# Kernel tuning notes

Hardware: AMD Instinct MI355X
Metric: run time of the kernel (lower is better)

The kernel has to match this reference:

```python
import jax, jax.numpy as jnp
import numpy as np


def setup_inputs() -> dict:
    key = jax.random.key(0)
    k1, k2, k3 = jax.random.split(key, 3)
    B, N, T, F = 4, 512, 64, 256
    x = jax.random.normal(k1, (B, N, T, F), dtype=jnp.float32)
    adj = jax.random.uniform(k2, (N, N), dtype=jnp.float32)
    # nn.Linear(F, F, bias=False) weight, layout [out, in]
    theta_w = jax.random.normal(k3, (F, F), dtype=jnp.float32) / np.float32(np.sqrt(F))
    return {"x": x, "adj": adj, "theta_w": theta_w}


def reference(x, adj, theta_w):
    # x: (B, N, T, F) -> out: (B, N, T, F). Dropout p=0 (eval mode).
    B, N, T, F = x.shape
    scale = np.float32(1.0 / np.sqrt(F))
    # fold time into batch: (B*T, N, F)
    xf = jnp.transpose(x, (0, 2, 1, 3)).reshape(B * T, N, F)
    # SAt: softmax((x x^T)/sqrt(F)); forward divides by sqrt(F) again
    score = jnp.einsum("bnf,bmf->bnm", xf, xf) * scale
    att = jax.nn.softmax(score, axis=-1) * scale  # (B*T, N, N)
    # adjacency-masked attention aggregation
    h = jnp.einsum("bnm,bmf->bnf", adj[None, :, :] * att, xf)  # (B*T, N, F)
    # Theta linear (no bias): y = h @ W^T
    y = jnp.einsum("bnf,of->bno", h, theta_w)
    y = y.reshape(B, T, N, F).transpose(0, 2, 1, 3)  # (B, N, T, F)
    return jax.nn.relu(y)
```

## Files before the change

### kernel.cpp

```cpp
#include <hip/hip_runtime.h>


typedef __attribute__((ext_vector_type(8))) _Float16 h16x8;
typedef __attribute__((ext_vector_type(4))) float f32x4;
typedef __attribute__((ext_vector_type(4))) unsigned short us4;
typedef __attribute__((ext_vector_type(8))) unsigned short us8;

#define MFMA16(a, b, c) __builtin_amdgcn_mfma_f32_16x16x32_f16((a), (b), (c), 0, 0, 0)

__device__ __forceinline__ unsigned short f2h(float f) {
    _Float16 h = (_Float16)f;
    return __builtin_bit_cast(unsigned short, h);
}
__device__ __forceinline__ void st4(unsigned short* p, unsigned short a, unsigned short b,
                                    unsigned short c, unsigned short d) {
    us4 v = {a, b, c, d};
    *(us4*)p = v;
}
__device__ __forceinline__ us8 pack8(float4 a, float4 b) {
    us8 v = {f2h(a.x), f2h(a.y), f2h(a.z), f2h(a.w), f2h(b.x), f2h(b.y), f2h(b.z), f2h(b.w)};
    return v;
}
__device__ __forceinline__ void gload16(const void* g, void* l) {
    __builtin_amdgcn_global_load_lds(
        (const __attribute__((address_space(1))) unsigned int*)g,
        (__attribute__((address_space(3))) unsigned int*)l, 16, 0, 0);
}

namespace {
constexpr int Nn = 512;
constexpr int TT = 64;
constexpr int FF = 256;
constexpr int TTFF = TT * FF;
constexpr int PLD = 40;
constexpr int XLD = 264;
constexpr float SCALE = 0.0625f;
constexpr float K2 = 0.09016844f;
constexpr float C2 = 24.525816f;
constexpr float CLMP = 15.9f;
constexpr size_t XH_ELEMS = (size_t)256 * 512 * 256;
constexpr size_t XT_ELEMS = (size_t)256 * 256 * 512;
constexpr size_t WH_ELEMS = 256 * 256;
constexpr size_t AJ_ELEMS = (size_t)2 * 16 * 8192;
constexpr int KLD = 264;
constexpr int TLD = 72;
constexpr int FPLD = 40;
constexpr int HLD = 256;
constexpr int WLD = 128;
}

__global__ __launch_bounds__(256, 4) void prepass(const float* __restrict__ x,
                                                  const float* __restrict__ W,
                                                  const float* __restrict__ adj,
                                                  unsigned short* __restrict__ xh,
                                                  unsigned short* __restrict__ xT2,
                                                  unsigned short* __restrict__ Wh,
                                                  unsigned short* __restrict__ adjL) {
    const int bid = blockIdx.x;
    const int t = threadIdx.x;
    if (bid >= 2056) {
        const int bid2 = bid - 2056;
        #pragma unroll
        for (int k = 0; k < 4; ++k) {
            const int U = bid2 * 1024 + k * 256 + t;
            const int qt  = U >> 14;
            const int t16 = (U >> 10) & 15;
            const int u   = U & 1023;
            const int half = u >> 9;
            const int wv   = (u >> 6) & 7;
            const int lv   = u & 63;
            const int lgv  = lv >> 4, lcv = lv & 15;
            us8 v;
            #pragma unroll
            for (int ee = 0; ee < 8; ++ee) {
                const int jt = ee >> 2, r = ee & 3;
                const int row = qt * 256 + wv * 32 + half * 16 + lgv * 4 + r;
                const int col = t16 * 32 + jt * 16 + lcv;
                v[ee] = f2h(adj[(size_t)row * Nn + col]);
            }
            *(us8*)&adjL[(size_t)U * 8] = v;
        }
        return;
    }
    if (bid >= 2048) {
        const int j = (bid - 2048) * 256 + t;
        #pragma unroll
        for (int k = 0; k < 4; ++k) {
            float4 a = *(const float4*)(W + j * 32 + k * 8);
            float4 b = *(const float4*)(W + j * 32 + k * 8 + 4);
            *(us8*)&Wh[j * 32 + k * 8] = pack8(a, b);
        }
        return;
    }
    __shared__ unsigned short tile[64 * XLD];
    const int bt = bid >> 3;
    const int nc = bid & 7;
    const int b = bt >> 6, tt = bt & 63;
    const int nbase = nc * 64;
    const float* xbt = x + (size_t)b * (Nn * TTFF) + (size_t)tt * FF;

    const int fb8 = (t & 31) * 8;
    const int rg = t >> 5;
    #pragma unroll
    for (int i = 0; i < 8; ++i) {
        const int rl = rg * 8 + i;
        const int n = nbase + rl;
        float4 a = *(const float4*)(xbt + (size_t)n * TTFF + fb8);
        float4 c = *(const float4*)(xbt + (size_t)n * TTFF + fb8 + 4);
        us8 v = pack8(a, c);
        *(us8*)&xh[((size_t)bt * Nn + n) * FF + (fb8 ^ (8 * (n & 7)))] = v;
        *(us8*)&tile[rl * XLD + fb8] = v;
    }
    __syncthreads();
    const int n0 = (t & 7) * 8;
    const int fr = t >> 3;
    #pragma unroll
    for (int j = 0; j < 8; ++j) {
        const int f = fr + 32 * j;
        const int g2 = 8 * ((f >> 1) & 3);
        const int n0p = (n0 & 32) | ((n0 & 24) ^ g2);
        us8 v;
        #pragma unroll
        for (int k = 0; k < 8; ++k) v[k] = tile[(n0p + k) * XLD + f];
        const int m = nbase + n0;
        *(us8*)&xT2[((size_t)bt * 16 + (m >> 5)) * 8192 + f * 32 + (m & 31)] = v;
    }
}

__global__ __launch_bounds__(512, 2) void gcn_main(float* __restrict__ out,
                                                   const unsigned short* __restrict__ xh,
                                                   const unsigned short* __restrict__ xT2,
                                                   const unsigned short* __restrict__ Wh,
                                                   const unsigned short* __restrict__ adjL) {
    __shared__ alignas(16) union {
        struct { unsigned short kt[2][32][256]; unsigned short vt[2][256][32];
                 unsigned short at[2][8192]; unsigned short pb[8][32][PLD]; } m;
        struct { unsigned short hb[256][264]; unsigned short wc[64][136]; } e;
    } sm;

    const int tid = threadIdx.x;
    const int w  = tid >> 6;
    const int l  = tid & 63;
    const int lg = l >> 4;
    const int lc = l & 15;
    const int fsw = 8 * (lc & 7);

    const int lb = (blockIdx.x & 7) * 64 + (blockIdx.x >> 3);
    const int bt = lb >> 1;
    const int qt = lb & 1;
    const int b  = bt >> 6;
    const int tt = bt & 63;
    const int qbase = qt * 256;

    const unsigned short* xhb = xh + (size_t)bt * (Nn * FF);
    const unsigned short* xTb = xT2 + (size_t)bt * (FF * Nn);
    const unsigned short* ajq = adjL + (size_t)qt * (16 * 8192);

    auto stage = [&](int u) {
        const int c = u & 1;
        const size_t off = (size_t)(u & 15) * 8192 + (size_t)tid * 8;
        unsigned short* ktd = &sm.m.kt[c][0][0] + (size_t)tid * 8;
        unsigned short* vtd = &sm.m.vt[c][0][0] + (size_t)tid * 8;
        unsigned short* atd = &sm.m.at[c][0]    + (size_t)tid * 8;
        gload16(&xhb[off],        ktd);
        gload16(&xhb[off + 4096], ktd + 4096);
        gload16(&xTb[off],        vtd);
        gload16(&xTb[off + 4096], vtd + 4096);
        gload16(&ajq[off],        atd);
        gload16(&ajq[off + 4096], atd + 4096);
    };

    stage(0);

    h16x8 qf[2][8];
    #pragma unroll
    for (int qs = 0; qs < 2; ++qs) {
        const unsigned short* qp = &xhb[(size_t)(qbase + 32 * w + 16 * qs + lc) * FF];
        #pragma unroll
        for (int ks = 0; ks < 8; ++ks) {
            us8 v = *(const us8*)(qp + ((ks * 32 + lg * 8) ^ fsw));
            qf[qs][ks] = __builtin_bit_cast(h16x8, v);
        }
    }

    f32x4 acc[2][16];
    #pragma unroll
    for (int q = 0; q < 2; ++q)
        #pragma unroll
        for (int i = 0; i < 16; ++i) { f32x4 z = {0.f, 0.f, 0.f, 0.f}; acc[q][i] = z; }
    float rs[2][4] = {{0.f,0.f,0.f,0.f},{0.f,0.f,0.f,0.f}};
    const int msw2 = 8 * ((lc >> 1) & 3);
    const int pwsw = 8 * ((lg >> 1) & 1);
    const int prsw = 8 * ((lc >> 3) & 1);

    for (int t = 0; t < 16; ++t) {
        const int c = t & 1;

        asm volatile("s_waitcnt vmcnt(0)" ::: "memory");
        __builtin_amdgcn_s_barrier();
        __builtin_amdgcn_sched_barrier(0);

        stage(t + 1);

        h16x8 a0 = *(const h16x8*)&sm.m.at[c][(w << 9) + l * 8];
        h16x8 a1 = *(const h16x8*)&sm.m.at[c][4096 + (w << 9) + l * 8];

        f32x4 s[2][2];
        #pragma unroll
        for (int qs = 0; qs < 2; ++qs)
            #pragma unroll
            for (int jt = 0; jt < 2; ++jt) { f32x4 z = {0.f,0.f,0.f,0.f}; s[qs][jt] = z; }
        __builtin_amdgcn_s_setprio(1);
        #pragma unroll
        for (int ks = 0; ks < 8; ++ks) {
            const int col = (ks * 32 + lg * 8) ^ fsw;
            h16x8 b0 = *(const h16x8*)&sm.m.kt[c][lc][col];
            h16x8 b1 = *(const h16x8*)&sm.m.kt[c][16 + lc][col];
            s[0][0] = MFMA16(qf[0][ks], b0, s[0][0]);
            s[0][1] = MFMA16(qf[0][ks], b1, s[0][1]);
            s[1][0] = MFMA16(qf[1][ks], b0, s[1][0]);
            s[1][1] = MFMA16(qf[1][ks], b1, s[1][1]);
        }
        __builtin_amdgcn_s_setprio(0);

        #pragma unroll
        for (int qs = 0; qs < 2; ++qs)
            #pragma unroll
            for (int jt = 0; jt < 2; ++jt)
                #pragma unroll
                for (int r = 0; r < 4; ++r) {
                    float p = exp2f(fminf(fmaf(s[qs][jt][r], K2, -C2), CLMP));
                    rs[qs][r] += p;
                    float av = (float)(qs ? a1[jt * 4 + r] : a0[jt * 4 + r]);
                    sm.m.pb[w][qs * 16 + 4 * lg + r][(jt * 16 + lc) ^ pwsw] = f2h(p * av);
                }
        h16x8 pa0 = *(const h16x8*)&sm.m.pb[w][lc][(lg * 8) ^ prsw];
        h16x8 pa1 = *(const h16x8*)&sm.m.pb[w][16 + lc][(lg * 8) ^ prsw];

        const int mcol = (lg * 8) ^ msw2;
        __builtin_amdgcn_s_setprio(1);
        #pragma unroll
        for (int ft = 0; ft < 16; ++ft) {
            h16x8 bv = *(const h16x8*)&sm.m.vt[c][ft * 16 + lc][mcol];
            acc[0][ft] = MFMA16(pa0, bv, acc[0][ft]);
            acc[1][ft] = MFMA16(pa1, bv, acc[1][ft]);
        }
        __builtin_amdgcn_s_setprio(0);
    }

    asm volatile("s_waitcnt vmcnt(0)" ::: "memory");
    __builtin_amdgcn_s_barrier();

    {
        #pragma unroll
        for (int qs = 0; qs < 2; ++qs) {
            float c0[4];
            #pragma unroll
            for (int r = 0; r < 4; ++r) {
                float t0 = rs[qs][r];
                t0 += __shfl_xor(t0, 1);
                t0 += __shfl_xor(t0, 2);
                t0 += __shfl_xor(t0, 4);
                t0 += __shfl_xor(t0, 8);
                c0[r] = SCALE / t0;
            }
            #pragma unroll
            for (int ft = 0; ft < 16; ++ft)
                #pragma unroll
                for (int r = 0; r < 4; ++r)
                    sm.e.hb[32 * w + 16 * qs + 4 * lg + r][ft * 16 + lc] =
                        f2h(acc[qs][ft][r] * c0[r]);
        }
    }

    #pragma unroll
    for (int ohh = 0; ohh < 4; ++ohh) {
        f32x4 y4[2][4];
        #pragma unroll
        for (int qs = 0; qs < 2; ++qs)
            #pragma unroll
            for (int i = 0; i < 4; ++i) { f32x4 z = {0.f, 0.f, 0.f, 0.f}; y4[qs][i] = z; }
        #pragma unroll
        for (int fh = 0; fh < 2; ++fh) {
            __syncthreads();
            {
                const int o  = tid >> 3;
                const int cc = (tid & 7) * 16;
                const unsigned short* gp = &Wh[(size_t)(ohh * 64 + o) * FF + fh * 128 + cc];
                *(us8*)&sm.e.wc[o][cc]     = *(const us8*)gp;
                *(us8*)&sm.e.wc[o][cc + 8] = *(const us8*)(gp + 8);
            }
            __syncthreads();
            h16x8 ha[2][4];
            #pragma unroll
            for (int qs = 0; qs < 2; ++qs)
                #pragma unroll
                for (int k2 = 0; k2 < 4; ++k2)
                    ha[qs][k2] = *(const h16x8*)
                        &sm.e.hb[32 * w + 16 * qs + lc][fh * 128 + k2 * 32 + lg * 8];
            #pragma unroll
            for (int ot = 0; ot < 4; ++ot) {
                #pragma unroll
                for (int k2 = 0; k2 < 4; ++k2) {
                    h16x8 bw = *(const h16x8*)&sm.e.wc[ot * 16 + lc][k2 * 32 + lg * 8];
                    y4[0][ot] = MFMA16(ha[0][k2], bw, y4[0][ot]);
                    y4[1][ot] = MFMA16(ha[1][k2], bw, y4[1][ot]);
                }
            }
        }
        #pragma unroll
        for (int qs = 0; qs < 2; ++qs)
            #pragma unroll
            for (int r = 0; r < 4; ++r) {
                const int row = qbase + 32 * w + 16 * qs + 4 * lg + r;
                float* op = &out[((size_t)(b * Nn + row) * TT + tt) * FF];
                #pragma unroll
                for (int ot = 0; ot < 4; ++ot) {
                    const int o = ohh * 64 + ot * 16 + lc;
                    float v = y4[qs][ot][r];
                    op[o] = v > 0.f ? v : 0.f;
                }
            }
    }
}

__global__ __launch_bounds__(256, 2) void gcn_fallback(const float* __restrict__ x,
                                                       const float* __restrict__ adj,
                                                       const float* __restrict__ W,
                                                       float* __restrict__ out) {
    __shared__ alignas(16) union {
        struct { unsigned short kt[64 * KLD]; unsigned short vt[256 * TLD];
                 unsigned short pb[4 * 32 * FPLD]; } m;
        struct { unsigned short hb[128 * HLD]; unsigned short wc[32 * WLD]; } e;
    } sm;

    const int tid = threadIdx.x;
    const int w  = tid >> 6;
    const int l  = tid & 63;
    const int lg = l >> 4;
    const int lc = l & 15;

    const int lb = (blockIdx.x & 7) * 128 + (blockIdx.x >> 3);
    const int bt = lb >> 2;
    const int qt = lb & 3;
    const int b  = bt >> 6;
    const int tt = bt & 63;
    const int qbase = qt * 128;

    const float* xbt = x + (size_t)b * (Nn * TTFF) + (size_t)tt * FF;

    h16x8 qf[2][8];
    #pragma unroll
    for (int qs = 0; qs < 2; ++qs) {
        const float* qp = xbt + (size_t)(qbase + 32 * w + 16 * qs + lc) * TTFF;
        #pragma unroll
        for (int ks = 0; ks < 8; ++ks) {
            float4 a = *(const float4*)(qp + ks * 32 + lg * 8);
            float4 c = *(const float4*)(qp + ks * 32 + lg * 8 + 4);
            h16x8 v;
            v[0] = (_Float16)(a.x * SCALE); v[1] = (_Float16)(a.y * SCALE);
            v[2] = (_Float16)(a.z * SCALE); v[3] = (_Float16)(a.w * SCALE);
            v[4] = (_Float16)(c.x * SCALE); v[5] = (_Float16)(c.y * SCALE);
            v[6] = (_Float16)(c.z * SCALE); v[7] = (_Float16)(c.w * SCALE);
            qf[qs][ks] = v;
        }
    }

    f32x4 acc[2][16];
    #pragma unroll
    for (int q = 0; q < 2; ++q)
        #pragma unroll
        for (int i = 0; i < 16; ++i) { f32x4 z = {0.f, 0.f, 0.f, 0.f}; acc[q][i] = z; }
    float mrow[2][4] = {{-1e30f,-1e30f,-1e30f,-1e30f},{-1e30f,-1e30f,-1e30f,-1e30f}};
    float lrow[2][4] = {{0.f,0.f,0.f,0.f},{0.f,0.f,0.f,0.f}};

    const int m0  = 4 * (tid >> 4);
    const int fb4 = 4 * (tid & 15);
    const int msw = m0 ^ (8 * (tid & 7));

    for (int kt2 = 0; kt2 < 8; ++kt2) {
        const int kbase = kt2 * 64;
        #pragma unroll
        for (int i = 0; i < 4; ++i) {
            const int f0 = fb4 + 64 * i;
            const float* p = xbt + (size_t)(kbase + m0) * TTFF + f0;
            float4 r0 = *(const float4*)(p);
            float4 r1 = *(const float4*)(p + TTFF);
            float4 r2 = *(const float4*)(p + 2 * TTFF);
            float4 r3 = *(const float4*)(p + 3 * TTFF);
            unsigned short a0=f2h(r0.x),a1=f2h(r0.y),a2=f2h(r0.z),a3=f2h(r0.w);
            unsigned short b0=f2h(r1.x),b1=f2h(r1.y),b2=f2h(r1.z),b3=f2h(r1.w);
            unsigned short c0=f2h(r2.x),c1=f2h(r2.y),c2=f2h(r2.z),c3=f2h(r2.w);
            unsigned short d0=f2h(r3.x),d1=f2h(r3.y),d2=f2h(r3.z),d3=f2h(r3.w);
            st4(&sm.m.kt[(m0 + 0) * KLD + f0], a0, a1, a2, a3);
            st4(&sm.m.kt[(m0 + 1) * KLD + f0], b0, b1, b2, b3);
            st4(&sm.m.kt[(m0 + 2) * KLD + f0], c0, c1, c2, c3);
            st4(&sm.m.kt[(m0 + 3) * KLD + f0], d0, d1, d2, d3);
            st4(&sm.m.vt[(f0 + 0) * TLD + msw], a0, b0, c0, d0);
            st4(&sm.m.vt[(f0 + 1) * TLD + msw], a1, b1, c1, d1);
            st4(&sm.m.vt[(f0 + 2) * TLD + msw], a2, b2, c2, d2);
            st4(&sm.m.vt[(f0 + 3) * TLD + msw], a3, b3, c3, d3);
        }
        __syncthreads();

        f32x4 s0[4], s1[4];
        #pragma unroll
        for (int jt = 0; jt < 4; ++jt) {
            f32x4 t0 = {0.f, 0.f, 0.f, 0.f}, t1 = {0.f, 0.f, 0.f, 0.f};
            #pragma unroll
            for (int ks = 0; ks < 8; ++ks) {
                h16x8 bf = *(const h16x8*)&sm.m.kt[(jt * 16 + lc) * KLD + ks * 32 + lg * 8];
                t0 = MFMA16(qf[0][ks], bf, t0);
                t1 = MFMA16(qf[1][ks], bf, t1);
            }
            s0[jt] = t0; s1[jt] = t1;
        }

        float resc[2][4];
        #pragma unroll
        for (int qs = 0; qs < 2; ++qs) {
            f32x4* s = qs ? s1 : s0;
            const int qrow0 = qbase + 32 * w + 16 * qs + 4 * lg;
            #pragma unroll
            for (int r = 0; r < 4; ++r) {
                float mx = fmaxf(fmaxf(s[0][r], s[1][r]), fmaxf(s[2][r], s[3][r]));
                mx = fmaxf(mx, __shfl_xor(mx, 1));
                mx = fmaxf(mx, __shfl_xor(mx, 2));
                mx = fmaxf(mx, __shfl_xor(mx, 4));
                mx = fmaxf(mx, __shfl_xor(mx, 8));
                float mnew = fmaxf(mrow[qs][r], mx);
                resc[qs][r] = exp2f((mrow[qs][r] - mnew) * 1.44269504f);
                mrow[qs][r] = mnew;
                float rss = 0.f;
                #pragma unroll
                for (int jt = 0; jt < 4; ++jt) {
                    float p = exp2f((s[jt][r] - mnew) * 1.44269504f);
                    rss += p;
                    s[jt][r] = p * adj[(qrow0 + r) * Nn + kbase + jt * 16 + lc];
                }
                rss += __shfl_xor(rss, 1);
                rss += __shfl_xor(rss, 2);
                rss += __shfl_xor(rss, 4);
                rss += __shfl_xor(rss, 8);
                lrow[qs][r] = lrow[qs][r] * resc[qs][r] + rss;
            }
        }
        #pragma unroll
        for (int qs = 0; qs < 2; ++qs)
            #pragma unroll
            for (int ft = 0; ft < 16; ++ft)
                #pragma unroll
                for (int r = 0; r < 4; ++r) acc[qs][ft][r] *= resc[qs][r];

        #pragma unroll
        for (int ks = 0; ks < 2; ++ks) {
            #pragma unroll
            for (int qs = 0; qs < 2; ++qs) {
                const f32x4* s = qs ? s1 : s0;
                #pragma unroll
                for (int jl = 0; jl < 2; ++jl)
                    #pragma unroll
                    for (int r = 0; r < 4; ++r)
                        sm.m.pb[(w * 32 + qs * 16 + 4 * lg + r) * FPLD + jl * 16 + lc] =
                            f2h(s[2 * ks + jl][r]);
            }
            h16x8 pa0 = *(const h16x8*)&sm.m.pb[(w * 32 + lc) * FPLD + lg * 8];
            h16x8 pa1 = *(const h16x8*)&sm.m.pb[(w * 32 + 16 + lc) * FPLD + lg * 8];
            #pragma unroll
            for (int ft = 0; ft < 16; ++ft) {
                const int f = ft * 16 + lc;
                const int ms = (ks * 32 + lg * 8) ^ (8 * ((4 * ft + (lc >> 2)) & 7));
                h16x8 bv = *(const h16x8*)&sm.m.vt[f * TLD + ms];
                acc[0][ft] = MFMA16(pa0, bv, acc[0][ft]);
                acc[1][ft] = MFMA16(pa1, bv, acc[1][ft]);
            }
        }
        __syncthreads();
    }

    {
        float c0[2][4];
        #pragma unroll
        for (int qs = 0; qs < 2; ++qs)
            #pragma unroll
            for (int r = 0; r < 4; ++r) c0[qs][r] = SCALE / lrow[qs][r];
        #pragma unroll
        for (int qs = 0; qs < 2; ++qs)
            #pragma unroll
            for (int ft = 0; ft < 16; ++ft)
                #pragma unroll
                for (int r = 0; r < 4; ++r) {
                    const int row = 32 * w + 16 * qs + 4 * lg + r;
                    const int col = (ft * 16 + lc) ^ (8 * ((4 * lg + r) & 7));
                    sm.e.hb[row * HLD + col] = f2h(acc[qs][ft][r] * c0[qs][r]);
                }
    }
    __syncthreads();

    f32x4 y[8][2][2];
    #pragma unroll
    for (int oh = 0; oh < 8; ++oh)
        #pragma unroll
        for (int qs = 0; qs < 2; ++qs)
            #pragma unroll
            for (int ot = 0; ot < 2; ++ot) { f32x4 z = {0.f,0.f,0.f,0.f}; y[oh][qs][ot] = z; }

    #pragma unroll
    for (int fh = 0; fh < 2; ++fh) {
        h16x8 ha[2][4];
        #pragma unroll
        for (int qs = 0; qs < 2; ++qs)
            #pragma unroll
            for (int k2 = 0; k2 < 4; ++k2) {
                const int row = 32 * w + 16 * qs + lc;
                const int col = (fh * 128 + k2 * 32 + lg * 8) ^ (8 * (lc & 7));
                ha[qs][k2] = *(const h16x8*)&sm.e.hb[row * HLD + col];
            }
        #pragma unroll
        for (int oh = 0; oh < 8; ++oh) {
            __syncthreads();
            {
                const int o  = tid >> 3;
                const int cb = (tid & 7) * 16;
                const float* gp = &W[(size_t)(oh * 32 + o) * FF + fh * 128 + cb];
                float4 v0 = *(const float4*)(gp);
                float4 v1 = *(const float4*)(gp + 4);
                float4 v2 = *(const float4*)(gp + 8);
                float4 v3 = *(const float4*)(gp + 12);
                const int sw = 16 * (o & 3);
                *(us8*)&sm.e.wc[o * WLD + (cb ^ sw)]       = pack8(v0, v1);
                *(us8*)&sm.e.wc[o * WLD + ((cb + 8) ^ sw)] = pack8(v2, v3);
            }
            __syncthreads();
            #pragma unroll
            for (int ot = 0; ot < 2; ++ot) {
                #pragma unroll
                for (int k2 = 0; k2 < 4; ++k2) {
                    const int row = ot * 16 + lc;
                    const int col = (k2 * 32 + lg * 8) ^ (16 * (lc & 3));
                    h16x8 bw = *(const h16x8*)&sm.e.wc[row * WLD + col];
                    y[oh][0][ot] = MFMA16(ha[0][k2], bw, y[oh][0][ot]);
                    y[oh][1][ot] = MFMA16(ha[1][k2], bw, y[oh][1][ot]);
                }
            }
        }
    }

    #pragma unroll
    for (int qs = 0; qs < 2; ++qs)
        #pragma unroll
        for (int r = 0; r < 4; ++r) {
            const int row = qbase + 32 * w + 16 * qs + 4 * lg + r;
            float* op = &out[((size_t)(b * Nn + row) * TT + tt) * FF];
            #pragma unroll
            for (int oh = 0; oh < 8; ++oh)
                #pragma unroll
                for (int ot = 0; ot < 2; ++ot) {
                    const int o = oh * 32 + ot * 16 + lc;
                    float v = y[oh][qs][ot][r];
                    op[o] = v > 0.f ? v : 0.f;
                }
        }
}

extern "C" void kernel_launch(void* const* d_in, const int* in_sizes, int n_in,
                              void* d_out, int out_size, void* d_ws, size_t ws_size,
                              hipStream_t stream) {
    const float* x   = (const float*)d_in[0];
    const float* adj = (const float*)d_in[1];
    const float* w   = (const float*)d_in[2];
    float* out       = (float*)d_out;
    (void)in_sizes; (void)n_in; (void)out_size;

    unsigned short* xh  = (unsigned short*)d_ws;
    unsigned short* xT2 = xh + XH_ELEMS;
    unsigned short* Wh  = xT2 + XT_ELEMS;
    unsigned short* aL  = Wh + WH_ELEMS;
    const size_t need = (XH_ELEMS + XT_ELEMS + WH_ELEMS + AJ_ELEMS) * sizeof(unsigned short);

    if (ws_size >= need) {
        prepass<<<dim3(2088), dim3(256), 0, stream>>>(x, w, adj, xh, xT2, Wh, aL);
        gcn_main<<<dim3(512), dim3(512), 0, stream>>>(out, xh, xT2, Wh, aL);
    } else {
        gcn_fallback<<<dim3(1024), dim3(256), 0, stream>>>(x, adj, w, out);
    }
}
```

Baseline: 176.0 us.

## Triple-buffer K/V staging, prefetch W through registers, and swizzle hb LDS

The K/V tiles in the main attention loop become triple-buffered and are issued two iterations ahead. The wait now uses a partial vmcnt instead of draining all loads, which is meant to hide global-load latency behind the MFMA work. The epilogue Theta GEMM now double-buffers 32-row W chunks and prefetches the next chunk into registers while the current one is computed, and XOR swizzles are added to the hb and pb LDS accesses to cut bank conflicts. The costs are more LDS per block, which may reduce occupancy, and more barriers in the epilogue because chunks are smaller.

Measured after the change: 189.1 us. +7.4%, slower.

```diff
diff --git a/kernel.cpp b/kernel.cpp
--- a/kernel.cpp
+++ b/kernel.cpp
@@ -133,9 +133,12 @@
                                                    const unsigned short* __restrict__ Wh,
                                                    const unsigned short* __restrict__ adjL) {
     __shared__ alignas(16) union {
-        struct { unsigned short kt[2][32][256]; unsigned short vt[2][256][32];
-                 unsigned short at[2][8192]; unsigned short pb[8][32][PLD]; } m;
-        struct { unsigned short hb[256][264]; unsigned short wc[64][136]; } e;
+        struct { unsigned short kt[3][32][256];
+                 unsigned short vt[3][256][32];
+                 unsigned short at[2][8192];
+                 unsigned short pb[8][32][PLD]; } m;
+        struct { unsigned short hb[256][264];
+                 unsigned short wc[2][32][136]; } e;
     } sm;
 
     const int tid = threadIdx.x;
@@ -156,32 +159,39 @@
     const unsigned short* xTb = xT2 + (size_t)bt * (FF * Nn);
     const unsigned short* ajq = adjL + (size_t)qt * (16 * 8192);
 
-    auto stage = [&](int u) {
-        const int c = u & 1;
+    h16x8 qf[2][8];
+    #pragma unroll
+    for (int qs = 0; qs < 2; ++qs) {
+        const unsigned short* qp = &xhb[(size_t)(qbase + 32 * w + 16 * qs + lc) * FF];
+        #pragma unroll
+        for (int ks = 0; ks < 8; ++ks) {
+            us8 v = *(const us8*)(qp + ((ks * 32 + lg * 8) ^ fsw));
+            qf[qs][ks] = __builtin_bit_cast(h16x8, v);
+        }
+    }
+    __builtin_amdgcn_sched_barrier(0);
+
+    auto stageK = [&](int u) {
+        const int c = u % 3;
         const size_t off = (size_t)(u & 15) * 8192 + (size_t)tid * 8;
         unsigned short* ktd = &sm.m.kt[c][0][0] + (size_t)tid * 8;
         unsigned short* vtd = &sm.m.vt[c][0][0] + (size_t)tid * 8;
-        unsigned short* atd = &sm.m.at[c][0]    + (size_t)tid * 8;
         gload16(&xhb[off],        ktd);
         gload16(&xhb[off + 4096], ktd + 4096);
         gload16(&xTb[off],        vtd);
         gload16(&xTb[off + 4096], vtd + 4096);
+    };
+    auto stageA = [&](int u) {
+        const int c = u & 1;
+        const size_t off = (size_t)(u & 15) * 8192 + (size_t)tid * 8;
+        unsigned short* atd = &sm.m.at[c][0] + (size_t)tid * 8;
         gload16(&ajq[off],        atd);
         gload16(&ajq[off + 4096], atd + 4096);
     };
 
-    stage(0);
-
-    h16x8 qf[2][8];
-    #pragma unroll
-    for (int qs = 0; qs < 2; ++qs) {
-        const unsigned short* qp = &xhb[(size_t)(qbase + 32 * w + 16 * qs + lc) * FF];
-        #pragma unroll
-        for (int ks = 0; ks < 8; ++ks) {
-            us8 v = *(const us8*)(qp + ((ks * 32 + lg * 8) ^ fsw));
-            qf[qs][ks] = __builtin_bit_cast(h16x8, v);
-        }
-    }
+    stageK(0);
+    stageA(0);
+    stageK(1);
 
     f32x4 acc[2][16];
     #pragma unroll
@@ -190,20 +200,21 @@
         for (int i = 0; i < 16; ++i) { f32x4 z = {0.f, 0.f, 0.f, 0.f}; acc[q][i] = z; }
     float rs[2][4] = {{0.f,0.f,0.f,0.f},{0.f,0.f,0.f,0.f}};
     const int msw2 = 8 * ((lc >> 1) & 3);
-    const int pwsw = 8 * ((lg >> 1) & 1);
-    const int prsw = 8 * ((lc >> 3) & 1);
+    const int pwsw = 16 * ((lg >> 1) & 1);
+    const int prsw = 16 * ((lc >> 3) & 1);
 
     for (int t = 0; t < 16; ++t) {
-        const int c = t & 1;
-
-        asm volatile("s_waitcnt vmcnt(0)" ::: "memory");
+        const int c = t % 3;
+
+        asm volatile("s_waitcnt vmcnt(4)" ::: "memory");
         __builtin_amdgcn_s_barrier();
         __builtin_amdgcn_sched_barrier(0);
 
-        stage(t + 1);
-
-        h16x8 a0 = *(const h16x8*)&sm.m.at[c][(w << 9) + l * 8];
-        h16x8 a1 = *(const h16x8*)&sm.m.at[c][4096 + (w << 9) + l * 8];
+        stageA(t + 1);
+        stageK(t + 2);
+
+        h16x8 a0 = *(const h16x8*)&sm.m.at[t & 1][(size_t)tid * 8];
+        h16x8 a1 = *(const h16x8*)&sm.m.at[t & 1][4096 + (size_t)tid * 8];
 
         f32x4 s[2][2];
         #pragma unroll
@@ -252,6 +263,7 @@
     __builtin_amdgcn_s_barrier();
 
     {
+        const int hws = 16 * ((lg >> 1) & 1);
         #pragma unroll
         for (int qs = 0; qs < 2; ++qs) {
             float c0[4];
@@ -268,59 +280,68 @@
             for (int ft = 0; ft < 16; ++ft)
                 #pragma unroll
                 for (int r = 0; r < 4; ++r)
-                    sm.e.hb[32 * w + 16 * qs + 4 * lg + r][ft * 16 + lc] =
+                    sm.e.hb[32 * w + 16 * qs + 4 * lg + r][(ft * 16 + lc) ^ hws] =
                         f2h(acc[qs][ft][r] * c0[r]);
         }
     }
 
-    #pragma unroll
-    for (int ohh = 0; ohh < 4; ++ohh) {
-        f32x4 y4[2][4];
-        #pragma unroll
-        for (int qs = 0; qs < 2; ++qs)
-            #pragma unroll
-            for (int i = 0; i < 4; ++i) { f32x4 z = {0.f, 0.f, 0.f, 0.f}; y4[qs][i] = z; }
-        #pragma unroll
-        for (int fh = 0; fh < 2; ++fh) {
-            __syncthreads();
-            {
-                const int o  = tid >> 3;
-                const int cc = (tid & 7) * 16;
-                const unsigned short* gp = &Wh[(size_t)(ohh * 64 + o) * FF + fh * 128 + cc];
-                *(us8*)&sm.e.wc[o][cc]     = *(const us8*)gp;
-                *(us8*)&sm.e.wc[o][cc + 8] = *(const us8*)(gp + 8);
-            }
-            __syncthreads();
-            h16x8 ha[2][4];
+    const int wo  = tid >> 4;
+    const int wcc = (tid & 15) * 8;
+    auto wld = [&](int ch) {
+        return *(const us8*)&Wh[(size_t)((ch >> 1) * 32 + wo) * FF + (ch & 1) * 128 + wcc];
+    };
+    const int hrsw = 16 * ((lc >> 3) & 1);
+
+    us8 wreg = wld(0);
+    *(us8*)&sm.e.wc[0][wo][wcc] = wreg;
+    wreg = wld(1);
+    __syncthreads();
+
+    f32x4 y4[2][2];
+    for (int ch = 0; ch < 16; ++ch) {
+        const int oq = ch >> 1, fh = ch & 1;
+        if (fh == 0) {
             #pragma unroll
             for (int qs = 0; qs < 2; ++qs)
                 #pragma unroll
-                for (int k2 = 0; k2 < 4; ++k2)
-                    ha[qs][k2] = *(const h16x8*)
-                        &sm.e.hb[32 * w + 16 * qs + lc][fh * 128 + k2 * 32 + lg * 8];
-            #pragma unroll
-            for (int ot = 0; ot < 4; ++ot) {
-                #pragma unroll
-                for (int k2 = 0; k2 < 4; ++k2) {
-                    h16x8 bw = *(const h16x8*)&sm.e.wc[ot * 16 + lc][k2 * 32 + lg * 8];
-                    y4[0][ot] = MFMA16(ha[0][k2], bw, y4[0][ot]);
-                    y4[1][ot] = MFMA16(ha[1][k2], bw, y4[1][ot]);
+                for (int ot = 0; ot < 2; ++ot) { f32x4 z = {0.f,0.f,0.f,0.f}; y4[qs][ot] = z; }
+        }
+        h16x8 ha[2][4];
+        #pragma unroll
+        for (int qs = 0; qs < 2; ++qs)
+            #pragma unroll
+            for (int k2 = 0; k2 < 4; ++k2)
+                ha[qs][k2] = *(const h16x8*)
+                    &sm.e.hb[32 * w + 16 * qs + lc][(fh * 128 + k2 * 32 + lg * 8) ^ hrsw];
+        #pragma unroll
+        for (int ot = 0; ot < 2; ++ot) {
+            #pragma unroll
+            for (int k2 = 0; k2 < 4; ++k2) {
+                h16x8 bw = *(const h16x8*)&sm.e.wc[ch & 1][ot * 16 + lc][k2 * 32 + lg * 8];
+                y4[0][ot] = MFMA16(ha[0][k2], bw, y4[0][ot]);
+                y4[1][ot] = MFMA16(ha[1][k2], bw, y4[1][ot]);
+            }
+        }
+        if (ch < 15) {
+            *(us8*)&sm.e.wc[(ch + 1) & 1][wo][wcc] = wreg;
+            if (ch < 14) wreg = wld(ch + 2);
+        }
+        __syncthreads();
+        if (fh == 1) {
+            #pragma unroll
+            for (int qs = 0; qs < 2; ++qs)
+                #pragma unroll
+                for (int r = 0; r < 4; ++r) {
+                    const int row = qbase + 32 * w + 16 * qs + 4 * lg + r;
+                    float* op = &out[((size_t)(b * Nn + row) * TT + tt) * FF];
+                    #pragma unroll
+                    for (int ot = 0; ot < 2; ++ot) {
+                        const int o = oq * 32 + ot * 16 + lc;
+                        float v = y4[qs][ot][r];
+                        op[o] = v > 0.f ? v : 0.f;
+                    }
                 }
-            }
-        }
-        #pragma unroll
-        for (int qs = 0; qs < 2; ++qs)
-            #pragma unroll
-            for (int r = 0; r < 4; ++r) {
-                const int row = qbase + 32 * w + 16 * qs + 4 * lg + r;
-                float* op = &out[((size_t)(b * Nn + row) * TT + tt) * FF];
-                #pragma unroll
-                for (int ot = 0; ot < 4; ++ot) {
-                    const int o = ohh * 64 + ot * 16 + lc;
-                    float v = y4[qs][ot][r];
-                    op[o] = v > 0.f ? v : 0.f;
-                }
-            }
+        }
     }
 }
 
```

## Split main kernel into 256-thread blocks of 128 queries, load adjacency from registers

Applied to the files above, without the earlier changes.

Restructures gcn_main so each block uses 4 waves covering 128 query rows instead of 8 waves covering 256, doubling the grid to 1024 blocks. Adjacency tiles are re-laid out in the prepass so each thread reads its 16 fp16 values directly from global memory into registers rather than staging them through LDS, which shrinks shared-memory use. The P-buffer swizzle is removed and its padding changed, and the epilogue is retiled to 32-column output chunks. The intent is better occupancy and less LDS pressure, at the cost of K/V tiles being loaded twice as often across blocks and possible new LDS bank conflicts.

After: 183.0 us. 1.04x slower.

```diff
diff --git a/kernel.cpp b/kernel.cpp
--- a/kernel.cpp
+++ b/kernel.cpp
@@ -32,7 +32,7 @@
 constexpr int TT = 64;
 constexpr int FF = 256;
 constexpr int TTFF = TT * FF;
-constexpr int PLD = 40;
+constexpr int PLD = 36;
 constexpr int XLD = 264;
 constexpr float SCALE = 0.0625f;
 constexpr float K2 = 0.09016844f;
@@ -41,7 +41,7 @@
 constexpr size_t XH_ELEMS = (size_t)256 * 512 * 256;
 constexpr size_t XT_ELEMS = (size_t)256 * 256 * 512;
 constexpr size_t WH_ELEMS = 256 * 256;
-constexpr size_t AJ_ELEMS = (size_t)2 * 16 * 8192;
+constexpr size_t AJ_ELEMS = (size_t)4 * 16 * 256 * 16;
 constexpr int KLD = 264;
 constexpr int TLD = 72;
 constexpr int FPLD = 40;
@@ -63,22 +63,21 @@
         #pragma unroll
         for (int k = 0; k < 4; ++k) {
             const int U = bid2 * 1024 + k * 256 + t;
-            const int qt  = U >> 14;
-            const int t16 = (U >> 10) & 15;
-            const int u   = U & 1023;
-            const int half = u >> 9;
-            const int wv   = (u >> 6) & 7;
-            const int lv   = u & 63;
-            const int lgv  = lv >> 4, lcv = lv & 15;
-            us8 v;
+            const int qb  = U >> 12;
+            const int t16 = (U >> 8) & 15;
+            const int tv  = U & 255;
+            const int wv  = tv >> 6, lv = tv & 63, lgv = lv >> 4, lcv = lv & 15;
+            us8 v0, v1;
             #pragma unroll
             for (int ee = 0; ee < 8; ++ee) {
                 const int jt = ee >> 2, r = ee & 3;
-                const int row = qt * 256 + wv * 32 + half * 16 + lgv * 4 + r;
-                const int col = t16 * 32 + jt * 16 + lcv;
-                v[ee] = f2h(adj[(size_t)row * Nn + col]);
-            }
-            *(us8*)&adjL[(size_t)U * 8] = v;
+                const int row0 = qb * 128 + wv * 32 + lgv * 4 + r;
+                const int col  = t16 * 32 + jt * 16 + lcv;
+                v0[ee] = f2h(adj[(size_t)row0 * Nn + col]);
+                v1[ee] = f2h(adj[(size_t)(row0 + 16) * Nn + col]);
+            }
+            *(us8*)&adjL[(size_t)U * 16]     = v0;
+            *(us8*)&adjL[(size_t)U * 16 + 8] = v1;
         }
         return;
     }
@@ -127,15 +126,15 @@
     }
 }
 
-__global__ __launch_bounds__(512, 2) void gcn_main(float* __restrict__ out,
+__global__ __launch_bounds__(256, 2) void gcn_main(float* __restrict__ out,
                                                    const unsigned short* __restrict__ xh,
                                                    const unsigned short* __restrict__ xT2,
                                                    const unsigned short* __restrict__ Wh,
                                                    const unsigned short* __restrict__ adjL) {
     __shared__ alignas(16) union {
         struct { unsigned short kt[2][32][256]; unsigned short vt[2][256][32];
-                 unsigned short at[2][8192]; unsigned short pb[8][32][PLD]; } m;
-        struct { unsigned short hb[256][264]; unsigned short wc[64][136]; } e;
+                 unsigned short pb[4][32][PLD]; } m;
+        struct { unsigned short hb[128][264]; unsigned short wc[32][136]; } e;
     } sm;
 
     const int tid = threadIdx.x;
@@ -145,32 +144,16 @@
     const int lc = l & 15;
     const int fsw = 8 * (lc & 7);
 
-    const int lb = (blockIdx.x & 7) * 64 + (blockIdx.x >> 3);
-    const int bt = lb >> 1;
-    const int qt = lb & 1;
+    const int lb = (blockIdx.x & 7) * 128 + (blockIdx.x >> 3);
+    const int bt = lb >> 2;
+    const int qb = lb & 3;
     const int b  = bt >> 6;
     const int tt = bt & 63;
-    const int qbase = qt * 256;
+    const int qbase = qb * 128;
 
     const unsigned short* xhb = xh + (size_t)bt * (Nn * FF);
     const unsigned short* xTb = xT2 + (size_t)bt * (FF * Nn);
-    const unsigned short* ajq = adjL + (size_t)qt * (16 * 8192);
-
-    auto stage = [&](int u) {
-        const int c = u & 1;
-        const size_t off = (size_t)(u & 15) * 8192 + (size_t)tid * 8;
-        unsigned short* ktd = &sm.m.kt[c][0][0] + (size_t)tid * 8;
-        unsigned short* vtd = &sm.m.vt[c][0][0] + (size_t)tid * 8;
-        unsigned short* atd = &sm.m.at[c][0]    + (size_t)tid * 8;
-        gload16(&xhb[off],        ktd);
-        gload16(&xhb[off + 4096], ktd + 4096);
-        gload16(&xTb[off],        vtd);
-        gload16(&xTb[off + 4096], vtd + 4096);
-        gload16(&ajq[off],        atd);
-        gload16(&ajq[off + 4096], atd + 4096);
-    };
-
-    stage(0);
+    const unsigned short* ajq = adjL + (size_t)qb * (16 * 256 * 16);
 
     h16x8 qf[2][8];
     #pragma unroll
@@ -182,6 +165,21 @@
             qf[qs][ks] = __builtin_bit_cast(h16x8, v);
         }
     }
+    __builtin_amdgcn_sched_barrier(0);
+
+    auto stage = [&](int u) {
+        const int c = u & 1;
+        const size_t off = (size_t)u * 8192 + (size_t)tid * 8;
+        unsigned short* ktd = &sm.m.kt[c][0][0] + (size_t)tid * 8;
+        unsigned short* vtd = &sm.m.vt[c][0][0] + (size_t)tid * 8;
+        #pragma unroll
+        for (int i = 0; i < 4; ++i) {
+            gload16(&xhb[off + i * 2048], ktd + i * 2048);
+            gload16(&xTb[off + i * 2048], vtd + i * 2048);
+        }
+    };
+
+    stage(0);
 
     f32x4 acc[2][16];
     #pragma unroll
@@ -190,8 +188,6 @@
         for (int i = 0; i < 16; ++i) { f32x4 z = {0.f, 0.f, 0.f, 0.f}; acc[q][i] = z; }
     float rs[2][4] = {{0.f,0.f,0.f,0.f},{0.f,0.f,0.f,0.f}};
     const int msw2 = 8 * ((lc >> 1) & 3);
-    const int pwsw = 8 * ((lg >> 1) & 1);
-    const int prsw = 8 * ((lc >> 3) & 1);
 
     for (int t = 0; t < 16; ++t) {
         const int c = t & 1;
@@ -200,10 +196,15 @@
         __builtin_amdgcn_s_barrier();
         __builtin_amdgcn_sched_barrier(0);
 
+        const unsigned short* ajp = ajq + ((size_t)t * 256 + tid) * 16;
+        us8 a0v = *(const us8*)(ajp);
+        us8 a1v = *(const us8*)(ajp + 8);
+        __builtin_amdgcn_sched_barrier(0);
+
         stage(t + 1);
 
-        h16x8 a0 = *(const h16x8*)&sm.m.at[c][(w << 9) + l * 8];
-        h16x8 a1 = *(const h16x8*)&sm.m.at[c][4096 + (w << 9) + l * 8];
+        h16x8 a0 = __builtin_bit_cast(h16x8, a0v);
+        h16x8 a1 = __builtin_bit_cast(h16x8, a1v);
 
         f32x4 s[2][2];
         #pragma unroll
@@ -232,10 +233,10 @@
                     float p = exp2f(fminf(fmaf(s[qs][jt][r], K2, -C2), CLMP));
                     rs[qs][r] += p;
                     float av = (float)(qs ? a1[jt * 4 + r] : a0[jt * 4 + r]);
-                    sm.m.pb[w][qs * 16 + 4 * lg + r][(jt * 16 + lc) ^ pwsw] = f2h(p * av);
-                }
-        h16x8 pa0 = *(const h16x8*)&sm.m.pb[w][lc][(lg * 8) ^ prsw];
-        h16x8 pa1 = *(const h16x8*)&sm.m.pb[w][16 + lc][(lg * 8) ^ prsw];
+                    sm.m.pb[w][qs * 16 + 4 * lg + r][jt * 16 + lc] = f2h(p * av);
+                }
+        h16x8 pa0 = *(const h16x8*)&sm.m.pb[w][lc][lg * 8];
+        h16x8 pa1 = *(const h16x8*)&sm.m.pb[w][16 + lc][lg * 8];
 
         const int mcol = (lg * 8) ^ msw2;
         __builtin_amdgcn_s_setprio(1);
@@ -274,19 +275,19 @@
     }
 
     #pragma unroll
-    for (int ohh = 0; ohh < 4; ++ohh) {
-        f32x4 y4[2][4];
-        #pragma unroll
-        for (int qs = 0; qs < 2; ++qs)
-            #pragma unroll
-            for (int i = 0; i < 4; ++i) { f32x4 z = {0.f, 0.f, 0.f, 0.f}; y4[qs][i] = z; }
+    for (int oh = 0; oh < 8; ++oh) {
+        f32x4 y4[2][2];
+        #pragma unroll
+        for (int qs = 0; qs < 2; ++qs)
+            #pragma unroll
+            for (int ot = 0; ot < 2; ++ot) { f32x4 z = {0.f, 0.f, 0.f, 0.f}; y4[qs][ot] = z; }
         #pragma unroll
         for (int fh = 0; fh < 2; ++fh) {
             __syncthreads();
             {
                 const int o  = tid >> 3;
                 const int cc = (tid & 7) * 16;
-                const unsigned short* gp = &Wh[(size_t)(ohh * 64 + o) * FF + fh * 128 + cc];
+                const unsigned short* gp = &Wh[(size_t)(oh * 32 + o) * FF + fh * 128 + cc];
                 *(us8*)&sm.e.wc[o][cc]     = *(const us8*)gp;
                 *(us8*)&sm.e.wc[o][cc + 8] = *(const us8*)(gp + 8);
             }
@@ -299,7 +300,7 @@
                     ha[qs][k2] = *(const h16x8*)
                         &sm.e.hb[32 * w + 16 * qs + lc][fh * 128 + k2 * 32 + lg * 8];
             #pragma unroll
-            for (int ot = 0; ot < 4; ++ot) {
+            for (int ot = 0; ot < 2; ++ot) {
                 #pragma unroll
                 for (int k2 = 0; k2 < 4; ++k2) {
                     h16x8 bw = *(const h16x8*)&sm.e.wc[ot * 16 + lc][k2 * 32 + lg * 8];
@@ -315,8 +316,8 @@
                 const int row = qbase + 32 * w + 16 * qs + 4 * lg + r;
                 float* op = &out[((size_t)(b * Nn + row) * TT + tt) * FF];
                 #pragma unroll
-                for (int ot = 0; ot < 4; ++ot) {
-                    const int o = ohh * 64 + ot * 16 + lc;
+                for (int ot = 0; ot < 2; ++ot) {
+                    const int o = oh * 32 + ot * 16 + lc;
                     float v = y4[qs][ot][r];
                     op[o] = v > 0.f ? v : 0.f;
                 }
@@ -579,8 +580,8 @@
     const size_t need = (XH_ELEMS + XT_ELEMS + WH_ELEMS + AJ_ELEMS) * sizeof(unsigned short);
 
     if (ws_size >= need) {
-        prepass<<<dim3(2088), dim3(256), 0, stream>>>(x, w, adj, xh, xT2, Wh, aL);
-        gcn_main<<<dim3(512), dim3(512), 0, stream>>>(out, xh, xT2, Wh, aL);
+        prepass<<<dim3(2072), dim3(256), 0, stream>>>(x, w, adj, xh, xT2, Wh, aL);
+        gcn_main<<<dim3(1024), dim3(256), 0, stream>>>(out, xh, xT2, Wh, aL);
     } else {
         gcn_fallback<<<dim3(1024), dim3(256), 0, stream>>>(x, adj, w, out);
     }
```

## Stage 64-key tiles per barrier and load adjacency directly into registers

Applied to the files above, without the earlier changes.

The main attention loop now stages 64 keys per iteration (8 iterations instead of 16), halving the number of barriers and wait points. The adjacency tile is no longer copied through shared memory; each wave reads its packed adjacency values from global memory straight into registers before issuing the next stage's async copies. The final stage is skipped instead of prefetching a wrapped tile. In exchange, shared-memory use for K/V doubles and the adjacency global reads sit on the critical path after each barrier, which may expose latency or affect occupancy.

Result: slower. 291.2 us (+65.5%).

```diff
diff --git a/kernel.cpp b/kernel.cpp
--- a/kernel.cpp
+++ b/kernel.cpp
@@ -133,8 +133,9 @@
                                                    const unsigned short* __restrict__ Wh,
                                                    const unsigned short* __restrict__ adjL) {
     __shared__ alignas(16) union {
-        struct { unsigned short kt[2][32][256]; unsigned short vt[2][256][32];
-                 unsigned short at[2][8192]; unsigned short pb[8][32][PLD]; } m;
+        struct { unsigned short kt[2][64][256];
+                 unsigned short vt[2][2][256][32];
+                 unsigned short pb[8][32][PLD]; } m;
         struct { unsigned short hb[256][264]; unsigned short wc[64][136]; } e;
     } sm;
 
@@ -156,22 +157,6 @@
     const unsigned short* xTb = xT2 + (size_t)bt * (FF * Nn);
     const unsigned short* ajq = adjL + (size_t)qt * (16 * 8192);
 
-    auto stage = [&](int u) {
-        const int c = u & 1;
-        const size_t off = (size_t)(u & 15) * 8192 + (size_t)tid * 8;
-        unsigned short* ktd = &sm.m.kt[c][0][0] + (size_t)tid * 8;
-        unsigned short* vtd = &sm.m.vt[c][0][0] + (size_t)tid * 8;
-        unsigned short* atd = &sm.m.at[c][0]    + (size_t)tid * 8;
-        gload16(&xhb[off],        ktd);
-        gload16(&xhb[off + 4096], ktd + 4096);
-        gload16(&xTb[off],        vtd);
-        gload16(&xTb[off + 4096], vtd + 4096);
-        gload16(&ajq[off],        atd);
-        gload16(&ajq[off + 4096], atd + 4096);
-    };
-
-    stage(0);
-
     h16x8 qf[2][8];
     #pragma unroll
     for (int qs = 0; qs < 2; ++qs) {
@@ -182,6 +167,21 @@
             qf[qs][ks] = __builtin_bit_cast(h16x8, v);
         }
     }
+    __builtin_amdgcn_sched_barrier(0);
+
+    auto stage = [&](int u) {
+        const int c = u & 1;
+        const size_t off = (size_t)u * 16384 + (size_t)tid * 8;
+        unsigned short* ktd = &sm.m.kt[c][0][0]    + (size_t)tid * 8;
+        unsigned short* vtd = &sm.m.vt[c][0][0][0] + (size_t)tid * 8;
+        #pragma unroll
+        for (int i = 0; i < 4; ++i) {
+            gload16(&xhb[off + i * 4096], ktd + i * 4096);
+            gload16(&xTb[off + i * 4096], vtd + i * 4096);
+        }
+    };
+
+    stage(0);
 
     f32x4 acc[2][16];
     #pragma unroll
@@ -193,62 +193,73 @@
     const int pwsw = 8 * ((lg >> 1) & 1);
     const int prsw = 8 * ((lc >> 3) & 1);
 
-    for (int t = 0; t < 16; ++t) {
-        const int c = t & 1;
+    for (int u = 0; u < 8; ++u) {
+        const int c = u & 1;
 
         asm volatile("s_waitcnt vmcnt(0)" ::: "memory");
         __builtin_amdgcn_s_barrier();
         __builtin_amdgcn_sched_barrier(0);
 
-        stage(t + 1);
-
-        h16x8 a0 = *(const h16x8*)&sm.m.at[c][(w << 9) + l * 8];
-        h16x8 a1 = *(const h16x8*)&sm.m.at[c][4096 + (w << 9) + l * 8];
-
-        f32x4 s[2][2];
-        #pragma unroll
-        for (int qs = 0; qs < 2; ++qs)
-            #pragma unroll
-            for (int jt = 0; jt < 2; ++jt) { f32x4 z = {0.f,0.f,0.f,0.f}; s[qs][jt] = z; }
-        __builtin_amdgcn_s_setprio(1);
-        #pragma unroll
-        for (int ks = 0; ks < 8; ++ks) {
-            const int col = (ks * 32 + lg * 8) ^ fsw;
-            h16x8 b0 = *(const h16x8*)&sm.m.kt[c][lc][col];
-            h16x8 b1 = *(const h16x8*)&sm.m.kt[c][16 + lc][col];
-            s[0][0] = MFMA16(qf[0][ks], b0, s[0][0]);
-            s[0][1] = MFMA16(qf[0][ks], b1, s[0][1]);
-            s[1][0] = MFMA16(qf[1][ks], b0, s[1][0]);
-            s[1][1] = MFMA16(qf[1][ks], b1, s[1][1]);
-        }
-        __builtin_amdgcn_s_setprio(0);
-
-        #pragma unroll
-        for (int qs = 0; qs < 2; ++qs)
-            #pragma unroll
-            for (int jt = 0; jt < 2; ++jt)
-                #pragma unroll
-                for (int r = 0; r < 4; ++r) {
-                    float p = exp2f(fminf(fmaf(s[qs][jt][r], K2, -C2), CLMP));
-                    rs[qs][r] += p;
-                    float av = (float)(qs ? a1[jt * 4 + r] : a0[jt * 4 + r]);
-                    sm.m.pb[w][qs * 16 + 4 * lg + r][(jt * 16 + lc) ^ pwsw] = f2h(p * av);
-                }
-        h16x8 pa0 = *(const h16x8*)&sm.m.pb[w][lc][(lg * 8) ^ prsw];
-        h16x8 pa1 = *(const h16x8*)&sm.m.pb[w][16 + lc][(lg * 8) ^ prsw];
-
-        const int mcol = (lg * 8) ^ msw2;
-        __builtin_amdgcn_s_setprio(1);
-        #pragma unroll
-        for (int ft = 0; ft < 16; ++ft) {
-            h16x8 bv = *(const h16x8*)&sm.m.vt[c][ft * 16 + lc][mcol];
-            acc[0][ft] = MFMA16(pa0, bv, acc[0][ft]);
-            acc[1][ft] = MFMA16(pa1, bv, acc[1][ft]);
-        }
-        __builtin_amdgcn_s_setprio(0);
-    }
-
-    asm volatile("s_waitcnt vmcnt(0)" ::: "memory");
+        us8 av[2][2];
+        #pragma unroll
+        for (int ss = 0; ss < 2; ++ss) {
+            const unsigned short* ap = ajq + (size_t)(2 * u + ss) * 8192 + (w << 9) + l * 8;
+            av[ss][0] = *(const us8*)(ap);
+            av[ss][1] = *(const us8*)(ap + 4096);
+        }
+        __builtin_amdgcn_sched_barrier(0);
+
+        if (u < 7) stage(u + 1);
+
+        #pragma unroll
+        for (int ss = 0; ss < 2; ++ss) {
+            h16x8 a0 = __builtin_bit_cast(h16x8, av[ss][0]);
+            h16x8 a1 = __builtin_bit_cast(h16x8, av[ss][1]);
+
+            f32x4 s[2][2];
+            #pragma unroll
+            for (int qs = 0; qs < 2; ++qs)
+                #pragma unroll
+                for (int jt = 0; jt < 2; ++jt) { f32x4 z = {0.f,0.f,0.f,0.f}; s[qs][jt] = z; }
+            __builtin_amdgcn_s_setprio(1);
+            #pragma unroll
+            for (int ks = 0; ks < 8; ++ks) {
+                const int col = (ks * 32 + lg * 8) ^ fsw;
+                h16x8 b0 = *(const h16x8*)&sm.m.kt[c][ss * 32 + lc][col];
+                h16x8 b1 = *(const h16x8*)&sm.m.kt[c][ss * 32 + 16 + lc][col];
+                s[0][0] = MFMA16(qf[0][ks], b0, s[0][0]);
+                s[0][1] = MFMA16(qf[0][ks], b1, s[0][1]);
+                s[1][0] = MFMA16(qf[1][ks], b0, s[1][0]);
+                s[1][1] = MFMA16(qf[1][ks], b1, s[1][1]);
+            }
+            __builtin_amdgcn_s_setprio(0);
+
+            #pragma unroll
+            for (int qs = 0; qs < 2; ++qs)
+                #pragma unroll
+                for (int jt = 0; jt < 2; ++jt)
+                    #pragma unroll
+                    for (int r = 0; r < 4; ++r) {
+                        float p = exp2f(fminf(fmaf(s[qs][jt][r], K2, -C2), CLMP));
+                        rs[qs][r] += p;
+                        float av2 = (float)(qs ? a1[jt * 4 + r] : a0[jt * 4 + r]);
+                        sm.m.pb[w][qs * 16 + 4 * lg + r][(jt * 16 + lc) ^ pwsw] = f2h(p * av2);
+                    }
+            h16x8 pa0 = *(const h16x8*)&sm.m.pb[w][lc][(lg * 8) ^ prsw];
+            h16x8 pa1 = *(const h16x8*)&sm.m.pb[w][16 + lc][(lg * 8) ^ prsw];
+
+            const int mcol = (lg * 8) ^ msw2;
+            __builtin_amdgcn_s_setprio(1);
+            #pragma unroll
+            for (int ft = 0; ft < 16; ++ft) {
+                h16x8 bv = *(const h16x8*)&sm.m.vt[c][ss][ft * 16 + lc][mcol];
+                acc[0][ft] = MFMA16(pa0, bv, acc[0][ft]);
+                acc[1][ft] = MFMA16(pa1, bv, acc[1][ft]);
+            }
+            __builtin_amdgcn_s_setprio(0);
+        }
+    }
+
     __builtin_amdgcn_s_barrier();
 
     {
```
